# Optimization experiments

Hardware: AMD Instinct MI355X
Metric: run time of the kernel (lower is better)

The kernel has to match this reference:

```python
import jax, jax.numpy as jnp
import numpy as np

EPS = 1e-5
SLOPE = 0.2


def _bn(x, g, b, m, v):
    # eval-mode BatchNorm1d over channel dim (last axis here)
    return (x - m) * (g * jax.lax.rsqrt(v + EPS)) + b


def _lrelu(x):
    return jnp.where(x >= 0, x, SLOPE * x)


def setup_inputs() -> dict:
    key = jax.random.key(0)
    ks = jax.random.split(key, 24)
    B, N = 16, 2048
    d = {
        "x_query": jax.random.normal(ks[0], (B, 2048), jnp.float32),
        "x_key": jax.random.normal(ks[1], (B, N, 512), jnp.float32),
        "W1": jax.random.normal(ks[2], (2048, 512), jnp.float32) * 0.02,
        "W2": jax.random.normal(ks[3], (512, 2048), jnp.float32) * 0.02,
        "W3": jax.random.normal(ks[4], (64, 512), jnp.float32) * 0.02,
        "W4": jax.random.normal(ks[5], (1, 64), jnp.float32) * 0.02,
    }
    for i, c in zip(range(4), (2048, 512, 64, 1)):
        d[f"g{i+1}"] = jax.random.uniform(ks[6 + 4 * i], (c,), jnp.float32, 0.5, 1.5)
        d[f"b{i+1}"] = jax.random.normal(ks[7 + 4 * i], (c,), jnp.float32) * 0.1
        d[f"m{i+1}"] = jax.random.normal(ks[8 + 4 * i], (c,), jnp.float32) * 0.1
        d[f"v{i+1}"] = jax.random.uniform(ks[9 + 4 * i], (c,), jnp.float32, 0.5, 1.5)
    return d


def reference(x_query, x_key, W1, W2, W3, W4,
              g1, b1, m1, v1, g2, b2, m2, v2,
              g3, b3, m3, v3, g4, b4, m4, v4):
    # values: [B, N, 2048]
    values = _lrelu(_bn(jnp.einsum('bnd,ed->bne', x_key, W1), g1, b1, m1, v1))
    features = values + x_query[:, None, :]
    s = _lrelu(_bn(jnp.einsum('bne,de->bnd', features, W2), g2, b2, m2, v2))
    s = _lrelu(_bn(jnp.einsum('bnd,kd->bnk', s, W3), g3, b3, m3, v3))
    s = _lrelu(_bn(jnp.einsum('bnk,ok->bno', s, W4), g4, b4, m4, v4))  # [B,N,1]
    scores = jax.nn.softmax(s[..., 0], axis=1)  # [B,N]
    feature = jnp.einsum('bne,bn->be', values, scores)  # softmax-weighted sum pool
    return feature
```

## Files before the change

kernel.cpp:

```cpp
#include <hip/hip_runtime.h>
#include <hip/hip_bf16.h>

typedef __bf16 bf16x8 __attribute__((ext_vector_type(8)));
typedef float f32x4 __attribute__((ext_vector_type(4)));
typedef __attribute__((address_space(3))) void lds_void_t;
typedef __attribute__((address_space(1))) void gbl_void_t;

#define LRELU(x) ((x) >= 0.f ? (x) : 0.2f * (x))

__device__ __forceinline__ void gload16(void* lds_uniform, const void* gsrc) {
    __builtin_amdgcn_global_load_lds((const gbl_void_t*)gsrc, (lds_void_t*)lds_uniform,
                                     16, 0, 0);
}

__device__ __forceinline__ unsigned short f2u(float f) {
    __hip_bfloat16 h = __float2bfloat16(f);
    return reinterpret_cast<unsigned short&>(h);
}

__global__ void cvt_f32_bf16(const float* __restrict__ in,
                             __hip_bfloat16* __restrict__ out, int n4) {
    int stride = gridDim.x * blockDim.x;
    for (int i = blockIdx.x * blockDim.x + threadIdx.x; i < n4; i += stride) {
        float4 v = reinterpret_cast<const float4*>(in)[i];
        ushort4 o;
        o.x = f2u(v.x); o.y = f2u(v.y); o.z = f2u(v.z); o.w = f2u(v.w);
        reinterpret_cast<ushort4*>(out)[i] = o;
    }
}


#define MMQ(AF, BF, IH, JH)                                                   \
    {                                                                         \
        _Pragma("unroll") for (int r = 0; r < 4; ++r) {                       \
            _Pragma("unroll") for (int c = 0; c < 2; ++c) {                   \
                _Pragma("unroll") for (int s = 0; s < 2; ++s) {               \
                    acc[(IH) * 4 + r][(JH) * 2 + c] =                         \
                        __builtin_amdgcn_mfma_f32_16x16x32_bf16(              \
                            AF[r][s], BF[c][s],                               \
                            acc[(IH) * 4 + r][(JH) * 2 + c], 0, 0, 0);        \
                }                                                             \
            }                                                                 \
        }                                                                     \
    }

#define LDA_(AF, BUF, IH)                                                     \
    {                                                                         \
        const __hip_bfloat16* _ab = sm + (BUF) * 32768 + wm * 8192;           \
        _Pragma("unroll") for (int r = 0; r < 4; ++r) {                       \
            const int _row = (IH) * 64 + r * 16 + lr;                         \
            _Pragma("unroll") for (int s = 0; s < 2; ++s) {                   \
                AF[r][s] = *reinterpret_cast<const bf16x8*>(                  \
                    _ab + _row * 64 + (((s * 4 + kg) ^ (lr & 7)) * 8));       \
            }                                                                 \
        }                                                                     \
    }

#define LDB_(BF, BUF, JH)                                                     \
    {                                                                         \
        const __hip_bfloat16* _bb =                                           \
            sm + (BUF) * 32768 + (2 + (wn >> 1)) * 8192;                      \
        _Pragma("unroll") for (int c = 0; c < 2; ++c) {                       \
            const int _row = (wn & 1) * 64 + ((JH) * 2 + c) * 16 + lr;        \
            _Pragma("unroll") for (int s = 0; s < 2; ++s) {                   \
                BF[c][s] = *reinterpret_cast<const bf16x8*>(                  \
                    _bb + _row * 64 + (((s * 4 + kg) ^ (lr & 7)) * 8));       \
            }                                                                 \
        }                                                                     \
    }

#define PH_MID                                                                \
    __builtin_amdgcn_s_barrier();                                             \
    asm volatile("s_waitcnt lgkmcnt(0)" ::: "memory");                        \
    __builtin_amdgcn_sched_barrier(0);                                        \
    __builtin_amdgcn_s_setprio(1);

#define PH_END                                                                \
    __builtin_amdgcn_s_setprio(0);                                            \
    __builtin_amdgcn_sched_barrier(0);                                        \
    __builtin_amdgcn_s_barrier();

template <int N, int K, int MODE>
__global__ __launch_bounds__(512, 1)
void gemm8p(const __hip_bfloat16* __restrict__ A,
            const __hip_bfloat16* __restrict__ Bw,
            const float* __restrict__ xq,
            __hip_bfloat16* __restrict__ out,
            const float* __restrict__ Gg, const float* __restrict__ Gb,
            const float* __restrict__ Gm, const float* __restrict__ Gv) {
    __shared__ __hip_bfloat16 sm[65536];

    const int nwg = gridDim.x;
    const int cpx = nwg >> 3;
    const int bid = blockIdx.x;
    const int orig = (bid & 7) * cpx + (bid >> 3);
    constexpr int NCB = N / 256;
    const int row0 = (orig / NCB) * 256;
    const int col0 = (orig % NCB) * 256;

    const int tid = threadIdx.x;
    const int lane = tid & 63;
    const int wv = tid >> 6;
    const int wm = wv >> 2, wn = wv & 3;
    const int lr = lane & 15, kg = lane >> 4;

    const int schunk = (tid & 7) ^ ((tid >> 3) & 7);
    const __hip_bfloat16* srcA0 = A + (size_t)(row0 + (tid >> 3)) * K + schunk * 8;
    const __hip_bfloat16* srcB0 = Bw + (size_t)(col0 + (tid >> 3)) * K + schunk * 8;
    constexpr size_t H = (size_t)128 * K;

    auto STG = [&](int buf, int region, const __hip_bfloat16* src) {
        __hip_bfloat16* l = sm + buf * 32768 + region * 8192 + wv * 512;
        gload16(l, src);
        gload16(l + 4096, src + (size_t)64 * K);
    };

    f32x4 acc[8][4];
#pragma unroll
    for (int i = 0; i < 8; ++i)
#pragma unroll
        for (int j = 0; j < 4; ++j) acc[i][j] = (f32x4){0.f, 0.f, 0.f, 0.f};

    bf16x8 af[4][2], bfrL[2][2], bfrH[2][2];

    STG(0, 0, srcA0);
    STG(0, 1, srcA0 + H);
    STG(0, 2, srcB0);
    STG(0, 3, srcB0 + H);
    STG(1, 2, srcB0 + 64);
    STG(1, 3, srcB0 + H + 64);
    asm volatile("s_waitcnt vmcnt(4)" ::: "memory");
    __builtin_amdgcn_s_barrier();

    constexpr int niter = K / 128;
    for (int it = 0; it < niter; ++it) {
        const int k0 = it * 128;
        const bool pf = (it + 1 < niter);

        LDA_(af, 0, 0);
        LDB_(bfrL, 0, 0);
        STG(1, 0, srcA0 + k0 + 64);
        PH_MID; MMQ(af, bfrL, 0, 0); PH_END;

        LDB_(bfrH, 0, 1);
        STG(1, 1, srcA0 + H + k0 + 64);
        PH_MID; MMQ(af, bfrH, 0, 1); PH_END;

        LDA_(af, 0, 1);
        if (pf) STG(0, 2, srcB0 + k0 + 128);
        PH_MID; MMQ(af, bfrH, 1, 1); PH_END;

        if (pf) {
            STG(0, 3, srcB0 + H + k0 + 128);
            asm volatile("s_waitcnt vmcnt(4)" ::: "memory");
        } else {
            asm volatile("s_waitcnt vmcnt(0)" ::: "memory");
        }
        PH_MID; MMQ(af, bfrL, 1, 0); PH_END;

        LDA_(af, 1, 0);
        LDB_(bfrL, 1, 0);
        if (pf) STG(0, 0, srcA0 + k0 + 128);
        PH_MID; MMQ(af, bfrL, 0, 0); PH_END;

        LDB_(bfrH, 1, 1);
        if (pf) STG(0, 1, srcA0 + H + k0 + 128);
        PH_MID; MMQ(af, bfrH, 0, 1); PH_END;

        LDA_(af, 1, 1);
        if (pf) STG(1, 2, srcB0 + k0 + 192);
        PH_MID; MMQ(af, bfrH, 1, 1); PH_END;

        if (pf) {
            STG(1, 3, srcB0 + H + k0 + 192);
            asm volatile("s_waitcnt vmcnt(4)" ::: "memory");
        } else {
            asm volatile("s_waitcnt vmcnt(0)" ::: "memory");
        }
        PH_MID; MMQ(af, bfrL, 1, 0); PH_END;
    }

    const int bq = row0 >> 11;
    float scl[4], tcn[4], xqv[4];
#pragma unroll
    for (int j = 0; j < 4; ++j) {
        const int c = col0 + wn * 64 + j * 16 + lr;
        scl[j] = Gg[c] * rsqrtf(Gv[c] + 1e-5f);
        tcn[j] = Gb[c] - Gm[c] * scl[j];
        xqv[j] = (MODE == 1) ? xq[bq * 2048 + c] : 0.f;
    }
#pragma unroll
    for (int i = 0; i < 8; ++i) {
#pragma unroll
        for (int rI = 0; rI < 4; ++rI) {
            const int r = row0 + wm * 128 + i * 16 + kg * 4 + rI;
            const size_t rowoff = (size_t)r * N + col0 + wn * 64 + lr;
#pragma unroll
            for (int j = 0; j < 4; ++j) {
                float val = acc[i][j][rI] * scl[j] + tcn[j];
                val = LRELU(val) + xqv[j];
                out[rowoff + j * 16] = __float2bfloat16(val);
            }
        }
    }
}

__global__ __launch_bounds__(256)
void gemm3_l4(const __hip_bfloat16* __restrict__ A,
              const __hip_bfloat16* __restrict__ W3b,
              const float* __restrict__ W4,
              const float* __restrict__ g3, const float* __restrict__ b3,
              const float* __restrict__ m3, const float* __restrict__ v3,
              const float* __restrict__ g4, const float* __restrict__ b4,
              const float* __restrict__ m4, const float* __restrict__ v4,
              float* __restrict__ logits) {
    const int lane = threadIdx.x & 63;
    const int wv = threadIdx.x >> 6;
    const int row0 = blockIdx.x * 128 + wv * 32;
    const int lr = lane & 15, kg = lane >> 4;

    f32x4 acc[2][4];
#pragma unroll
    for (int i = 0; i < 2; ++i)
#pragma unroll
        for (int j = 0; j < 4; ++j) acc[i][j] = (f32x4){0.f, 0.f, 0.f, 0.f};

    for (int k = 0; k < 512; k += 32) {
        const int kk = k + kg * 8;
        bf16x8 a[2], b[4];
#pragma unroll
        for (int i = 0; i < 2; ++i)
            a[i] = *reinterpret_cast<const bf16x8*>(A + (size_t)(row0 + i * 16 + lr) * 512 + kk);
#pragma unroll
        for (int j = 0; j < 4; ++j)
            b[j] = *reinterpret_cast<const bf16x8*>(W3b + (size_t)(j * 16 + lr) * 512 + kk);
#pragma unroll
        for (int i = 0; i < 2; ++i)
#pragma unroll
            for (int j = 0; j < 4; ++j)
                acc[i][j] = __builtin_amdgcn_mfma_f32_16x16x32_bf16(a[i], b[j], acc[i][j], 0, 0, 0);
    }

    const float sc4 = g4[0] * rsqrtf(v4[0] + 1e-5f);
    const float tc4 = b4[0] - m4[0] * sc4;
#pragma unroll
    for (int i = 0; i < 2; ++i) {
        float t[4] = {0.f, 0.f, 0.f, 0.f};
#pragma unroll
        for (int j = 0; j < 4; ++j) {
            const int c = j * 16 + lr;
            const float sc = g3[c] * rsqrtf(v3[c] + 1e-5f);
            const float tc = b3[c] - m3[c] * sc;
            const float w4c = W4[c];
#pragma unroll
            for (int rI = 0; rI < 4; ++rI) {
                float v = acc[i][j][rI] * sc + tc;
                t[rI] += LRELU(v) * w4c;
            }
        }
#pragma unroll
        for (int m = 1; m < 16; m <<= 1)
#pragma unroll
            for (int rI = 0; rI < 4; ++rI) t[rI] += __shfl_xor(t[rI], m, 64);
        if (lr == 0) {
#pragma unroll
            for (int rI = 0; rI < 4; ++rI) {
                float lg = t[rI] * sc4 + tc4;
                logits[row0 + i * 16 + kg * 4 + rI] = LRELU(lg);
            }
        }
    }
}

__global__ void softmax2048(const float* __restrict__ logits, float* __restrict__ scores) {
    __shared__ float sh[2048];
    __shared__ float red[256];
    const int b = blockIdx.x, tid = threadIdx.x;
    float lmax = -1e30f;
#pragma unroll
    for (int it = 0; it < 8; ++it) {
        const int n = tid + it * 256;
        float v = logits[b * 2048 + n];
        sh[n] = v;
        lmax = fmaxf(lmax, v);
    }
    red[tid] = lmax;
    __syncthreads();
    for (int s = 128; s > 0; s >>= 1) {
        if (tid < s) red[tid] = fmaxf(red[tid], red[tid + s]);
        __syncthreads();
    }
    const float gmax = red[0];
    __syncthreads();
    float lsum = 0.f;
#pragma unroll
    for (int it = 0; it < 8; ++it) {
        const int n = tid + it * 256;
        float e = expf(sh[n] - gmax);
        sh[n] = e;
        lsum += e;
    }
    red[tid] = lsum;
    __syncthreads();
    for (int s = 128; s > 0; s >>= 1) {
        if (tid < s) red[tid] += red[tid + s];
        __syncthreads();
    }
    const float inv = 1.f / red[0];
#pragma unroll
    for (int it = 0; it < 8; ++it) {
        const int n = tid + it * 256;
        scores[b * 2048 + n] = sh[n] * inv;
    }
}

__global__ void pool_partial(const __hip_bfloat16* __restrict__ feats,
                             const float* __restrict__ scores,
                             float* __restrict__ partial) {
    const int b = blockIdx.y, nc = blockIdx.x;
    const int e0 = threadIdx.x * 8;
    float acc[8] = {0, 0, 0, 0, 0, 0, 0, 0};
    const size_t base = ((size_t)b * 2048 + nc * 64) * 2048;
    for (int i = 0; i < 64; ++i) {
        const float sc = scores[b * 2048 + nc * 64 + i];
        bf16x8 v = *reinterpret_cast<const bf16x8*>(feats + base + (size_t)i * 2048 + e0);
#pragma unroll
        for (int j = 0; j < 8; ++j) acc[j] += sc * (float)v[j];
    }
    float* p = partial + ((size_t)(b * 32 + nc)) * 2048 + e0;
#pragma unroll
    for (int j = 0; j < 8; ++j) p[j] = acc[j];
}

__global__ void pool_reduce(const float* __restrict__ partial,
                            const float* __restrict__ xq,
                            float* __restrict__ out) {
    const int i = blockIdx.x * blockDim.x + threadIdx.x;
    const int b = i >> 11, e = i & 2047;
    float s = 0.f;
#pragma unroll
    for (int nc = 0; nc < 32; ++nc) s += partial[((size_t)(b * 32 + nc)) * 2048 + e];
    out[i] = s - xq[i];
}

extern "C" void kernel_launch(void* const* d_in, const int* in_sizes, int n_in,
                              void* d_out, int out_size, void* d_ws, size_t ws_size,
                              hipStream_t stream) {
    const float* xq = (const float*)d_in[0];
    const float* xk = (const float*)d_in[1];
    const float* W1 = (const float*)d_in[2];
    const float* W2 = (const float*)d_in[3];
    const float* W3 = (const float*)d_in[4];
    const float* W4 = (const float*)d_in[5];
    const float* g1 = (const float*)d_in[6], *b1 = (const float*)d_in[7];
    const float* m1 = (const float*)d_in[8], *v1 = (const float*)d_in[9];
    const float* g2 = (const float*)d_in[10], *b2 = (const float*)d_in[11];
    const float* m2 = (const float*)d_in[12], *v2 = (const float*)d_in[13];
    const float* g3 = (const float*)d_in[14], *b3 = (const float*)d_in[15];
    const float* m3 = (const float*)d_in[16], *v3 = (const float*)d_in[17];
    const float* g4 = (const float*)d_in[18], *b4 = (const float*)d_in[19];
    const float* m4 = (const float*)d_in[20], *v4 = (const float*)d_in[21];

    const int M = 32768;

    char* ws = (char*)d_ws;
    size_t off = 0;
    auto alloc = [&](size_t bytes) {
        void* p = ws + off;
        off += (bytes + 255) & ~(size_t)255;
        return p;
    };
    __hip_bfloat16* xkb   = (__hip_bfloat16*)alloc((size_t)M * 512 * 2);
    __hip_bfloat16* w1b   = (__hip_bfloat16*)alloc((size_t)2048 * 512 * 2);
    __hip_bfloat16* w2b   = (__hip_bfloat16*)alloc((size_t)512 * 2048 * 2);
    __hip_bfloat16* w3b   = (__hip_bfloat16*)alloc((size_t)64 * 512 * 2);
    __hip_bfloat16* featb = (__hip_bfloat16*)alloc((size_t)M * 2048 * 2);
    __hip_bfloat16* s2b   = (__hip_bfloat16*)alloc((size_t)M * 512 * 2);
    float* logits         = (float*)alloc((size_t)M * 4);
    float* scores         = (float*)alloc((size_t)16 * 2048 * 4);
    float* partial        = (float*)alloc((size_t)16 * 32 * 2048 * 4);

    cvt_f32_bf16<<<4096, 256, 0, stream>>>(xk, xkb, M * 512 / 4);
    cvt_f32_bf16<<<1024, 256, 0, stream>>>(W1, w1b, 2048 * 512 / 4);
    cvt_f32_bf16<<<1024, 256, 0, stream>>>(W2, w2b, 512 * 2048 / 4);
    cvt_f32_bf16<<<32, 256, 0, stream>>>(W3, w3b, 64 * 512 / 4);

    gemm8p<2048, 512, 1><<<1024, 512, 0, stream>>>(
        xkb, w1b, xq, featb, g1, b1, m1, v1);

    gemm8p<512, 2048, 2><<<256, 512, 0, stream>>>(
        featb, w2b, nullptr, s2b, g2, b2, m2, v2);

    gemm3_l4<<<256, 256, 0, stream>>>(s2b, w3b, W4,
                                      g3, b3, m3, v3, g4, b4, m4, v4, logits);

    softmax2048<<<16, 256, 0, stream>>>(logits, scores);

    pool_partial<<<dim3(32, 16), 256, 0, stream>>>(featb, scores, partial);
    pool_reduce<<<128, 256, 0, stream>>>(partial, xq, (float*)d_out);
}
```

Measured before the change: 214.7 us.

## Double-buffer A fragments and drop per-phase lgkmcnt waits in GEMM main loop

```diff
diff --git a/kernel.cpp b/kernel.cpp
--- a/kernel.cpp
+++ b/kernel.cpp
@@ -69,20 +69,16 @@
         }                                                                     \
     }
 
-#define PH_MID                                                                \
-    __builtin_amdgcn_s_barrier();                                             \
-    asm volatile("s_waitcnt lgkmcnt(0)" ::: "memory");                        \
-    __builtin_amdgcn_sched_barrier(0);                                        \
-    __builtin_amdgcn_s_setprio(1);
-
-#define PH_END                                                                \
-    __builtin_amdgcn_s_setprio(0);                                            \
-    __builtin_amdgcn_sched_barrier(0);                                        \
-    __builtin_amdgcn_s_barrier();
+#define SCHED __builtin_amdgcn_sched_barrier(0)
+#define BAR __builtin_amdgcn_s_barrier()
+#define PRIO1 __builtin_amdgcn_s_setprio(1)
+#define PRIO0 __builtin_amdgcn_s_setprio(0)
+#define VMC4 asm volatile("s_waitcnt vmcnt(4)" ::: "memory")
+#define VMC0 asm volatile("s_waitcnt vmcnt(0)" ::: "memory")
 
 template <int N, int K, int MODE>
 __global__ __launch_bounds__(512, 1)
-void gemm8p(const __hip_bfloat16* __restrict__ A,
+void gemm9p(const __hip_bfloat16* __restrict__ A,
             const __hip_bfloat16* __restrict__ Bw,
             const float* __restrict__ xq,
             __hip_bfloat16* __restrict__ out,
@@ -121,7 +117,7 @@
 #pragma unroll
         for (int j = 0; j < 4; ++j) acc[i][j] = (f32x4){0.f, 0.f, 0.f, 0.f};
 
-    bf16x8 af[4][2], bfrL[2][2], bfrH[2][2];
+    bf16x8 afA[4][2], afB[4][2], bL[2][2], bH[2][2];
 
     STG(0, 0, srcA0);
     STG(0, 1, srcA0 + H);
@@ -129,55 +125,48 @@
     STG(0, 3, srcB0 + H);
     STG(1, 2, srcB0 + 64);
     STG(1, 3, srcB0 + H + 64);
-    asm volatile("s_waitcnt vmcnt(4)" ::: "memory");
-    __builtin_amdgcn_s_barrier();
+    VMC4;
+    BAR;
+    LDA_(afA, 0, 0);
 
     constexpr int niter = K / 128;
     for (int it = 0; it < niter; ++it) {
         const int k0 = it * 128;
         const bool pf = (it + 1 < niter);
 
-        LDA_(af, 0, 0);
-        LDB_(bfrL, 0, 0);
         STG(1, 0, srcA0 + k0 + 64);
-        PH_MID; MMQ(af, bfrL, 0, 0); PH_END;
-
-        LDB_(bfrH, 0, 1);
+        LDB_(bL, 0, 0);
+        LDB_(bH, 0, 1);
+        SCHED; PRIO1; MMQ(afA, bL, 0, 0); PRIO0; SCHED; BAR;
+
         STG(1, 1, srcA0 + H + k0 + 64);
-        PH_MID; MMQ(af, bfrH, 0, 1); PH_END;
-
-        LDA_(af, 0, 1);
+        LDA_(afB, 0, 1);
+        SCHED; PRIO1; MMQ(afA, bH, 0, 1); PRIO0; SCHED; BAR;
+
         if (pf) STG(0, 2, srcB0 + k0 + 128);
-        PH_MID; MMQ(af, bfrH, 1, 1); PH_END;
-
-        if (pf) {
-            STG(0, 3, srcB0 + H + k0 + 128);
-            asm volatile("s_waitcnt vmcnt(4)" ::: "memory");
-        } else {
-            asm volatile("s_waitcnt vmcnt(0)" ::: "memory");
-        }
-        PH_MID; MMQ(af, bfrL, 1, 0); PH_END;
-
-        LDA_(af, 1, 0);
-        LDB_(bfrL, 1, 0);
+        SCHED; PRIO1; MMQ(afB, bH, 1, 1); PRIO0; SCHED; BAR;
+
+        if (pf) { STG(0, 3, srcB0 + H + k0 + 128); VMC4; } else { VMC0; }
+        BAR;
+        LDA_(afA, 1, 0);
+        SCHED; PRIO1; MMQ(afB, bL, 1, 0); PRIO0; SCHED; BAR;
+
         if (pf) STG(0, 0, srcA0 + k0 + 128);
-        PH_MID; MMQ(af, bfrL, 0, 0); PH_END;
-
-        LDB_(bfrH, 1, 1);
+        LDB_(bL, 1, 0);
+        LDB_(bH, 1, 1);
+        SCHED; PRIO1; MMQ(afA, bL, 0, 0); PRIO0; SCHED; BAR;
+
         if (pf) STG(0, 1, srcA0 + H + k0 + 128);
-        PH_MID; MMQ(af, bfrH, 0, 1); PH_END;
-
-        LDA_(af, 1, 1);
+        LDA_(afB, 1, 1);
+        SCHED; PRIO1; MMQ(afA, bH, 0, 1); PRIO0; SCHED; BAR;
+
         if (pf) STG(1, 2, srcB0 + k0 + 192);
-        PH_MID; MMQ(af, bfrH, 1, 1); PH_END;
-
-        if (pf) {
-            STG(1, 3, srcB0 + H + k0 + 192);
-            asm volatile("s_waitcnt vmcnt(4)" ::: "memory");
-        } else {
-            asm volatile("s_waitcnt vmcnt(0)" ::: "memory");
-        }
-        PH_MID; MMQ(af, bfrL, 1, 0); PH_END;
+        SCHED; PRIO1; MMQ(afB, bH, 1, 1); PRIO0; SCHED; BAR;
+
+        if (pf) { STG(1, 3, srcB0 + H + k0 + 192); VMC4; } else { VMC0; }
+        BAR;
+        if (pf) LDA_(afA, 0, 0);
+        SCHED; PRIO1; MMQ(afB, bL, 1, 0); PRIO0; SCHED; BAR;
     }
 
     const int bq = row0 >> 11;
@@ -385,10 +374,10 @@
     cvt_f32_bf16<<<1024, 256, 0, stream>>>(W2, w2b, 512 * 2048 / 4);
     cvt_f32_bf16<<<32, 256, 0, stream>>>(W3, w3b, 64 * 512 / 4);
 
-    gemm8p<2048, 512, 1><<<1024, 512, 0, stream>>>(
+    gemm9p<2048, 512, 1><<<1024, 512, 0, stream>>>(
         xkb, w1b, xq, featb, g1, b1, m1, v1);
 
-    gemm8p<512, 2048, 2><<<256, 512, 0, stream>>>(
+    gemm9p<512, 2048, 2><<<256, 512, 0, stream>>>(
         featb, w2b, nullptr, s2b, g2, b2, m2, v2);
 
     gemm3_l4<<<256, 256, 0, stream>>>(s2b, w3b, W4,
```

New measurement: 237.4 us. 1.11x slower.

## Fuse x_key fp32-to-bf16 conversion into GEMM1 A-tile staging; merge weight casts

Applied to the files above, without the earlier changes.

```diff
diff --git a/kernel.cpp b/kernel.cpp
--- a/kernel.cpp
+++ b/kernel.cpp
@@ -18,14 +18,23 @@
     return reinterpret_cast<unsigned short&>(h);
 }
 
-__global__ void cvt_f32_bf16(const float* __restrict__ in,
-                             __hip_bfloat16* __restrict__ out, int n4) {
-    int stride = gridDim.x * blockDim.x;
-    for (int i = blockIdx.x * blockDim.x + threadIdx.x; i < n4; i += stride) {
-        float4 v = reinterpret_cast<const float4*>(in)[i];
-        ushort4 o;
-        o.x = f2u(v.x); o.y = f2u(v.y); o.z = f2u(v.z); o.w = f2u(v.w);
-        reinterpret_cast<ushort4*>(out)[i] = o;
+__global__ void cvt_w(const float* __restrict__ a, __hip_bfloat16* __restrict__ oa, int na,
+                      const float* __restrict__ b, __hip_bfloat16* __restrict__ ob, int nb,
+                      const float* __restrict__ c, __hip_bfloat16* __restrict__ oc, int nc) {
+    const int stride = gridDim.x * blockDim.x;
+    const int total = na + nb + nc;
+    for (int i = blockIdx.x * blockDim.x + threadIdx.x; i < total; i += stride) {
+        const float* s; __hip_bfloat16* o; int j = i;
+        if (j < na) { s = a; o = oa; }
+        else {
+            j -= na;
+            if (j < nb) { s = b; o = ob; }
+            else { j -= nb; s = c; o = oc; }
+        }
+        float4 v = reinterpret_cast<const float4*>(s)[j];
+        ushort4 u;
+        u.x = f2u(v.x); u.y = f2u(v.y); u.z = f2u(v.z); u.w = f2u(v.w);
+        reinterpret_cast<ushort4*>(o)[j] = u;
     }
 }
 
@@ -80,9 +89,10 @@
     __builtin_amdgcn_sched_barrier(0);                                        \
     __builtin_amdgcn_s_barrier();
 
-template <int N, int K, int MODE>
+template <int N, int K, int MODE, int ASRC>
 __global__ __launch_bounds__(512, 1)
 void gemm8p(const __hip_bfloat16* __restrict__ A,
+            const float* __restrict__ Af,
             const __hip_bfloat16* __restrict__ Bw,
             const float* __restrict__ xq,
             __hip_bfloat16* __restrict__ out,
@@ -106,6 +116,7 @@
 
     const int schunk = (tid & 7) ^ ((tid >> 3) & 7);
     const __hip_bfloat16* srcA0 = A + (size_t)(row0 + (tid >> 3)) * K + schunk * 8;
+    const float* srcAf = Af + (size_t)(row0 + (tid >> 3)) * K + schunk * 8;
     const __hip_bfloat16* srcB0 = Bw + (size_t)(col0 + (tid >> 3)) * K + schunk * 8;
     constexpr size_t H = (size_t)128 * K;
 
@@ -114,6 +125,25 @@
         gload16(l, src);
         gload16(l + 4096, src + (size_t)64 * K);
     };
+    auto STG_A32 = [&](int buf, int region, const float* src) {
+        __hip_bfloat16* l = sm + buf * 32768 + region * 8192 + tid * 8;
+#pragma unroll
+        for (int g = 0; g < 2; ++g) {
+            const float* s = src + g * (size_t)64 * K;
+            float4 v0 = *reinterpret_cast<const float4*>(s);
+            float4 v1 = *reinterpret_cast<const float4*>(s + 4);
+            bf16x8 r;
+            r[0] = (__bf16)v0.x; r[1] = (__bf16)v0.y;
+            r[2] = (__bf16)v0.z; r[3] = (__bf16)v0.w;
+            r[4] = (__bf16)v1.x; r[5] = (__bf16)v1.y;
+            r[6] = (__bf16)v1.z; r[7] = (__bf16)v1.w;
+            *reinterpret_cast<bf16x8*>(l + g * 4096) = r;
+        }
+    };
+    auto STG_A = [&](int buf, int region, int elemoff) {
+        if constexpr (ASRC == 1) STG_A32(buf, region, srcAf + elemoff);
+        else STG(buf, region, srcA0 + elemoff);
+    };
 
     f32x4 acc[8][4];
 #pragma unroll
@@ -123,13 +153,14 @@
 
     bf16x8 af[4][2], bfrL[2][2], bfrH[2][2];
 
-    STG(0, 0, srcA0);
-    STG(0, 1, srcA0 + H);
+    STG_A(0, 0, 0);
+    STG_A(0, 1, (int)H);
     STG(0, 2, srcB0);
     STG(0, 3, srcB0 + H);
     STG(1, 2, srcB0 + 64);
     STG(1, 3, srcB0 + H + 64);
     asm volatile("s_waitcnt vmcnt(4)" ::: "memory");
+    asm volatile("s_waitcnt lgkmcnt(0)" ::: "memory");
     __builtin_amdgcn_s_barrier();
 
     constexpr int niter = K / 128;
@@ -139,11 +170,11 @@
 
         LDA_(af, 0, 0);
         LDB_(bfrL, 0, 0);
-        STG(1, 0, srcA0 + k0 + 64);
+        STG_A(1, 0, k0 + 64);
         PH_MID; MMQ(af, bfrL, 0, 0); PH_END;
 
         LDB_(bfrH, 0, 1);
-        STG(1, 1, srcA0 + H + k0 + 64);
+        STG_A(1, 1, (int)H + k0 + 64);
         PH_MID; MMQ(af, bfrH, 0, 1); PH_END;
 
         LDA_(af, 0, 1);
@@ -160,11 +191,11 @@
 
         LDA_(af, 1, 0);
         LDB_(bfrL, 1, 0);
-        if (pf) STG(0, 0, srcA0 + k0 + 128);
+        if (pf) STG_A(0, 0, k0 + 128);
         PH_MID; MMQ(af, bfrL, 0, 0); PH_END;
 
         LDB_(bfrH, 1, 1);
-        if (pf) STG(0, 1, srcA0 + H + k0 + 128);
+        if (pf) STG_A(0, 1, (int)H + k0 + 128);
         PH_MID; MMQ(af, bfrH, 0, 1); PH_END;
 
         LDA_(af, 1, 1);
@@ -370,7 +401,6 @@
         off += (bytes + 255) & ~(size_t)255;
         return p;
     };
-    __hip_bfloat16* xkb   = (__hip_bfloat16*)alloc((size_t)M * 512 * 2);
     __hip_bfloat16* w1b   = (__hip_bfloat16*)alloc((size_t)2048 * 512 * 2);
     __hip_bfloat16* w2b   = (__hip_bfloat16*)alloc((size_t)512 * 2048 * 2);
     __hip_bfloat16* w3b   = (__hip_bfloat16*)alloc((size_t)64 * 512 * 2);
@@ -380,16 +410,16 @@
     float* scores         = (float*)alloc((size_t)16 * 2048 * 4);
     float* partial        = (float*)alloc((size_t)16 * 32 * 2048 * 4);
 
-    cvt_f32_bf16<<<4096, 256, 0, stream>>>(xk, xkb, M * 512 / 4);
-    cvt_f32_bf16<<<1024, 256, 0, stream>>>(W1, w1b, 2048 * 512 / 4);
-    cvt_f32_bf16<<<1024, 256, 0, stream>>>(W2, w2b, 512 * 2048 / 4);
-    cvt_f32_bf16<<<32, 256, 0, stream>>>(W3, w3b, 64 * 512 / 4);
-
-    gemm8p<2048, 512, 1><<<1024, 512, 0, stream>>>(
-        xkb, w1b, xq, featb, g1, b1, m1, v1);
-
-    gemm8p<512, 2048, 2><<<256, 512, 0, stream>>>(
-        featb, w2b, nullptr, s2b, g2, b2, m2, v2);
+    cvt_w<<<1024, 256, 0, stream>>>(
+        W1, w1b, 2048 * 512 / 4,
+        W2, w2b, 512 * 2048 / 4,
+        W3, w3b, 64 * 512 / 4);
+
+    gemm8p<2048, 512, 1, 1><<<1024, 512, 0, stream>>>(
+        nullptr, xk, w1b, xq, featb, g1, b1, m1, v1);
+
+    gemm8p<512, 2048, 2, 0><<<256, 512, 0, stream>>>(
+        featb, nullptr, w2b, nullptr, s2b, g2, b2, m2, v2);
 
     gemm3_l4<<<256, 256, 0, stream>>>(s2b, w3b, W4,
                                       g3, b3, m3, v3, g4, b4, m4, v4, logits);
```

After: 218.8 us. Within noise of the previous version (+1.9%).

## Fuse fp32-to-bf16 conversion launches and stage gemm3 operands through LDS

Applied to the files above, without the earlier changes.

```diff
diff --git a/kernel.cpp b/kernel.cpp
--- a/kernel.cpp
+++ b/kernel.cpp
@@ -18,14 +18,28 @@
     return reinterpret_cast<unsigned short&>(h);
 }
 
-__global__ void cvt_f32_bf16(const float* __restrict__ in,
-                             __hip_bfloat16* __restrict__ out, int n4) {
-    int stride = gridDim.x * blockDim.x;
-    for (int i = blockIdx.x * blockDim.x + threadIdx.x; i < n4; i += stride) {
-        float4 v = reinterpret_cast<const float4*>(in)[i];
-        ushort4 o;
-        o.x = f2u(v.x); o.y = f2u(v.y); o.z = f2u(v.z); o.w = f2u(v.w);
-        reinterpret_cast<ushort4*>(out)[i] = o;
+__global__ void cvt_fused(const float* __restrict__ a, __hip_bfloat16* __restrict__ oa, int na,
+                          const float* __restrict__ b, __hip_bfloat16* __restrict__ ob, int nb,
+                          const float* __restrict__ c, __hip_bfloat16* __restrict__ oc, int nc,
+                          const float* __restrict__ d, __hip_bfloat16* __restrict__ od, int nd) {
+    const int stride = gridDim.x * blockDim.x;
+    const int total = na + nb + nc + nd;
+    for (int i = blockIdx.x * blockDim.x + threadIdx.x; i < total; i += stride) {
+        const float* s; __hip_bfloat16* o; int j = i;
+        if (j < na) { s = a; o = oa; }
+        else {
+            j -= na;
+            if (j < nb) { s = b; o = ob; }
+            else {
+                j -= nb;
+                if (j < nc) { s = c; o = oc; }
+                else { j -= nc; s = d; o = od; }
+            }
+        }
+        float4 v = reinterpret_cast<const float4*>(s)[j];
+        ushort4 u;
+        u.x = f2u(v.x); u.y = f2u(v.y); u.z = f2u(v.z); u.w = f2u(v.w);
+        reinterpret_cast<ushort4*>(o)[j] = u;
     }
 }
 
@@ -205,7 +219,7 @@
     }
 }
 
-__global__ __launch_bounds__(256)
+__global__ __launch_bounds__(256, 2)
 void gemm3_l4(const __hip_bfloat16* __restrict__ A,
               const __hip_bfloat16* __restrict__ W3b,
               const float* __restrict__ W4,
@@ -214,11 +228,29 @@
               const float* __restrict__ g4, const float* __restrict__ b4,
               const float* __restrict__ m4, const float* __restrict__ v4,
               float* __restrict__ logits) {
-    const int lane = threadIdx.x & 63;
-    const int wv = threadIdx.x >> 6;
-    const int row0 = blockIdx.x * 128 + wv * 32;
+    __shared__ __hip_bfloat16 lA[128 * 32];
+    __shared__ __hip_bfloat16 lB[64 * 520];
+    const int tid = threadIdx.x;
+    const int lane = tid & 63;
+    const int wv = tid >> 6;
+    const int row0 = blockIdx.x * 128;
     const int lr = lane & 15, kg = lane >> 4;
 
+#pragma unroll
+    for (int p = 0; p < 16; ++p) {
+        const int idx = tid * 8 + p * 2048;
+        const int r = idx >> 9, c = idx & 511;
+        bf16x8 v = *reinterpret_cast<const bf16x8*>(W3b + idx);
+        *reinterpret_cast<bf16x8*>(&lB[r * 520 + c]) = v;
+    }
+
+    const int schunk = (lane & 3) ^ ((lane >> 3) & 3);
+    const __hip_bfloat16* Ag = A + (size_t)(row0 + wv * 32 + (lane >> 2)) * 512 + schunk * 8;
+    __hip_bfloat16* lAp = lA + wv * 1024;
+
+    const int koff = ((kg ^ ((lr >> 1) & 3)) << 3);
+    const int aoff = (wv * 32 + lr) * 32 + koff;
+
     f32x4 acc[2][4];
 #pragma unroll
     for (int i = 0; i < 2; ++i)
@@ -226,19 +258,23 @@
         for (int j = 0; j < 4; ++j) acc[i][j] = (f32x4){0.f, 0.f, 0.f, 0.f};
 
     for (int k = 0; k < 512; k += 32) {
-        const int kk = k + kg * 8;
+        gload16(lAp,       Ag + k);
+        gload16(lAp + 512, Ag + k + (size_t)16 * 512);
+        __syncthreads();
+
         bf16x8 a[2], b[4];
 #pragma unroll
         for (int i = 0; i < 2; ++i)
-            a[i] = *reinterpret_cast<const bf16x8*>(A + (size_t)(row0 + i * 16 + lr) * 512 + kk);
+            a[i] = *reinterpret_cast<const bf16x8*>(lA + aoff + i * 512);
 #pragma unroll
         for (int j = 0; j < 4; ++j)
-            b[j] = *reinterpret_cast<const bf16x8*>(W3b + (size_t)(j * 16 + lr) * 512 + kk);
+            b[j] = *reinterpret_cast<const bf16x8*>(&lB[(j * 16 + lr) * 520 + k + kg * 8]);
 #pragma unroll
         for (int i = 0; i < 2; ++i)
 #pragma unroll
             for (int j = 0; j < 4; ++j)
                 acc[i][j] = __builtin_amdgcn_mfma_f32_16x16x32_bf16(a[i], b[j], acc[i][j], 0, 0, 0);
+        __syncthreads();
     }
 
     const float sc4 = g4[0] * rsqrtf(v4[0] + 1e-5f);
@@ -266,7 +302,7 @@
 #pragma unroll
             for (int rI = 0; rI < 4; ++rI) {
                 float lg = t[rI] * sc4 + tc4;
-                logits[row0 + i * 16 + kg * 4 + rI] = LRELU(lg);
+                logits[row0 + wv * 32 + i * 16 + kg * 4 + rI] = LRELU(lg);
             }
         }
     }
@@ -380,10 +416,11 @@
     float* scores         = (float*)alloc((size_t)16 * 2048 * 4);
     float* partial        = (float*)alloc((size_t)16 * 32 * 2048 * 4);
 
-    cvt_f32_bf16<<<4096, 256, 0, stream>>>(xk, xkb, M * 512 / 4);
-    cvt_f32_bf16<<<1024, 256, 0, stream>>>(W1, w1b, 2048 * 512 / 4);
-    cvt_f32_bf16<<<1024, 256, 0, stream>>>(W2, w2b, 512 * 2048 / 4);
-    cvt_f32_bf16<<<32, 256, 0, stream>>>(W3, w3b, 64 * 512 / 4);
+    cvt_fused<<<4096, 256, 0, stream>>>(
+        xk, xkb, M * 512 / 4,
+        W1, w1b, 2048 * 512 / 4,
+        W2, w2b, 512 * 2048 / 4,
+        W3, w3b, 64 * 512 / 4);
 
     gemm8p<2048, 512, 1><<<1024, 512, 0, stream>>>(
         xkb, w1b, xq, featb, g1, b1, m1, v1);
```

New measurement: 205.1 us (median of 2 runs). 1.05x faster.
